# Optimization experiments

Measured on AMD Instinct MI355X. Metric: run time of the kernel, lower is better.

The kernel has to match this reference:

```python
import jax, jax.numpy as jnp
import numpy as np

K_BASE = 8
K_MAX = 20
NUM_GROUPS = 16  # min(32, 64 // 4)
EPS = 1e-5


def _knn_idx_adaptive(x, mask, k_base=K_BASE, k_max=K_MAX):
    # x: [B, N, D] float, mask: [B, N] bool. Returns idx: [B, N, k_max] int32.
    B, N, D = x.shape
    x2 = jnp.sum(x * x, axis=-1, keepdims=True)              # [B, N, 1]
    dist2 = x2 + x2.transpose(0, 2, 1) - 2.0 * jnp.einsum('bnd,bmd->bnm', x, x)
    dist2 = jnp.clip(dist2, 0.0)
    valid = mask[:, :, None] & mask[:, None, :]
    eye = jnp.eye(N, dtype=bool)[None]
    dist2 = jnp.where(valid & ~eye, dist2, jnp.inf)
    counts = mask.sum(axis=1)                                 # [B]
    k_per = jnp.clip(jnp.sqrt(counts.astype(jnp.float32) / 50.0) * k_base,
                     k_base, k_max).astype(jnp.int32)         # truncation == torch .long()
    k_global = jnp.minimum(k_max, jnp.maximum(1, counts.min() - 1))
    _, idx = jax.lax.top_k(-dist2, k_max)                     # [B, N, k_max]
    first_valid = jnp.argmax(mask, axis=1)                    # [B]
    cols = jnp.arange(k_max)[None, None, :]
    k_eff = jnp.minimum(k_per, k_global)[:, None, None]
    # cols < k_eff: true top-k neighbors; [k_eff, k_global): repeat first valid; >= k_global: pad 0
    idx = jnp.where(cols < k_eff, idx,
                    jnp.where(cols < k_global, first_valid[:, None, None], 0))
    return idx


def _group_norm(h, gamma, beta, num_groups=NUM_GROUPS, eps=EPS):
    # h: [..., C]
    shp = h.shape
    C = shp[-1]
    hg = h.reshape(shp[:-1] + (num_groups, C // num_groups))
    mu = hg.mean(axis=-1, keepdims=True)
    var = hg.var(axis=-1, keepdims=True)
    hg = (hg - mu) * jax.lax.rsqrt(var + eps)
    return hg.reshape(shp) * gamma + beta


def setup_inputs() -> dict:
    key = jax.random.key(0)
    kx, kl, k1, k2 = jax.random.split(key, 4)
    B, N, D, C = 16, 1024, 64, 64
    x = jax.random.normal(kx, (B, N, D), dtype=jnp.float32)
    lengths = jax.random.randint(kl, (B,), 256, N + 1)
    mask = jnp.arange(N)[None, :] < lengths[:, None]          # [B, N] bool
    W1 = jax.random.normal(k1, (2 * D, C), dtype=jnp.float32) / np.sqrt(2 * D)
    b1 = jnp.zeros((C,), dtype=jnp.float32)
    gamma = jnp.ones((C,), dtype=jnp.float32)
    beta = jnp.zeros((C,), dtype=jnp.float32)
    W2 = jax.random.normal(k2, (C, C), dtype=jnp.float32) / np.sqrt(C)
    b2 = jnp.zeros((C,), dtype=jnp.float32)
    return {"x": x, "mask": mask, "W1": W1, "b1": b1,
            "gamma": gamma, "beta": beta, "W2": W2, "b2": b2}


def reference(x, mask, W1, b1, gamma, beta, W2, b2):
    B, N, D = x.shape
    idx = _knn_idx_adaptive(x, mask)                          # [B, N, k]
    k = idx.shape[-1]
    x_nb = jnp.take_along_axis(x[:, :, None, :].repeat(1, axis=2),
                               idx[..., None], axis=1) if False else \
        x[jnp.arange(B)[:, None, None], idx]                  # [B, N, k, D]
    x_i = jnp.broadcast_to(x[:, :, None, :], (B, N, k, D))
    edge = jnp.concatenate([x_i, x_nb - x_i], axis=-1)        # [B, N, k, 2D]
    h = jax.nn.relu(_group_norm(edge @ W1 + b1, gamma, beta)) # [B, N, k, C]
    h = h @ W2 + b2
    out = h.max(axis=2)                                       # [B, N, C]
    return out * mask[..., None].astype(out.dtype)
```

## Files before the change

### kernel.cpp

```cpp
#include <hip/hip_runtime.h>
#include <stdint.h>

#define BB 16
#define NN 1024
#define DD 64
#define CC 64
#define KMAX 20
#define ROWS 8

typedef unsigned long long u64;
typedef float f32x2 __attribute__((ext_vector_type(2)));
typedef float f32x4v __attribute__((ext_vector_type(4)));
typedef short bf16x8 __attribute__((ext_vector_type(8)));

__device__ inline u64 umin64(u64 a, u64 b) { return a < b ? a : b; }

__device__ inline unsigned f2bf(float f) {
    unsigned u = __float_as_uint(f);
    return (u + 0x7FFFu + ((u >> 16) & 1u)) >> 16;
}

__device__ inline bf16x8 pack8(const float4 a, const float4 b) {
    union { unsigned u[4]; bf16x8 v; } r;
    r.u[0] = f2bf(a.x) | (f2bf(a.y) << 16);
    r.u[1] = f2bf(a.z) | (f2bf(a.w) << 16);
    r.u[2] = f2bf(b.x) | (f2bf(b.y) << 16);
    r.u[3] = f2bf(b.z) | (f2bf(b.w) << 16);
    return r.v;
}

struct bfpair { bf16x8 hi, lo; };
__device__ __forceinline__ bfpair split8(const float v[8]) {
    union { unsigned u[4]; bf16x8 x; } H, L;
#pragma unroll
    for (int i = 0; i < 4; ++i) {
        unsigned h0 = f2bf(v[2 * i]), h1 = f2bf(v[2 * i + 1]);
        float r0 = v[2 * i] - __uint_as_float(h0 << 16);
        float r1 = v[2 * i + 1] - __uint_as_float(h1 << 16);
        H.u[i] = h0 | (h1 << 16);
        L.u[i] = f2bf(r0) | (f2bf(r1) << 16);
    }
    bfpair r; r.hi = H.x; r.lo = L.x; return r;
}

__device__ inline void gn4(float4& h, const float4 g, const float4 be) {
    float mu = (h.x + h.y + h.z + h.w) * 0.25f;
    float dx = h.x - mu, dy = h.y - mu, dz = h.z - mu, dw = h.w - mu;
    float var = (dx * dx + dy * dy + dz * dz + dw * dw) * 0.25f;
    float rs = __builtin_amdgcn_rsqf(var + 1e-5f);
    h.x = fmaxf(fmaf(dx * rs, g.x, be.x), 0.f);
    h.y = fmaxf(fmaf(dy * rs, g.y, be.y), 0.f);
    h.z = fmaxf(fmaf(dz * rs, g.z, be.z), 0.f);
    h.w = fmaxf(fmaf(dw * rs, g.w, be.w), 0.f);
}

__global__ __launch_bounds__(256) void k1_feats(const float* __restrict__ x,
                                                const float* __restrict__ W1,
                                                const float* __restrict__ b1,
                                                float* __restrict__ base,
                                                float* __restrict__ fb,
                                                float* __restrict__ x2,
                                                float* __restrict__ xT,
                                                const void* __restrict__ maskp,
                                                int* __restrict__ counts,
                                                int* __restrict__ keff) {
    __shared__ float sXT[64][65];
    __shared__ int scnt[BB];
    int w = threadIdx.x >> 6, lane = threadIdx.x & 63;
    int lg = lane >> 4, lr = lane & 15;
    int p0 = blockIdx.x * 64;
    int pw0 = p0 + w * 16;

    float av[8];
    bfpair A[2];
    {
        const float* xr = x + (size_t)(pw0 + lr) * DD;
#pragma unroll
        for (int kt = 0; kt < 2; ++kt) {
            float4 a0 = *(const float4*)(xr + kt * 32 + lg * 8);
            float4 a1 = *(const float4*)(xr + kt * 32 + lg * 8 + 4);
            av[0] = a0.x; av[1] = a0.y; av[2] = a0.z; av[3] = a0.w;
            av[4] = a1.x; av[5] = a1.y; av[6] = a1.z; av[7] = a1.w;
            A[kt] = split8(av);
        }
    }
    bfpair Wa[4][2], Wb[4][2];
#pragma unroll
    for (int nt = 0; nt < 4; ++nt)
#pragma unroll
        for (int kt = 0; kt < 2; ++kt) {
            const float* wpa = W1 + (size_t)(kt * 32 + lg * 8) * CC + nt * 16 + lr;
            float wv[8];
#pragma unroll
            for (int e = 0; e < 8; ++e) wv[e] = wpa[e * CC];
            Wa[nt][kt] = split8(wv);
            const float* wpb = wpa + (size_t)DD * CC;
#pragma unroll
            for (int e = 0; e < 8; ++e) wv[e] = wpb[e * CC];
            Wb[nt][kt] = split8(wv);
        }

    f32x4v P[4], Q[4];
#pragma unroll
    for (int nt = 0; nt < 4; ++nt) { P[nt] = (f32x4v){0,0,0,0}; Q[nt] = (f32x4v){0,0,0,0}; }
#pragma unroll
    for (int nt = 0; nt < 4; ++nt)
#pragma unroll
        for (int kt = 0; kt < 2; ++kt) {
            P[nt] = __builtin_amdgcn_mfma_f32_16x16x32_bf16(A[kt].hi, Wa[nt][kt].hi, P[nt], 0, 0, 0);
            P[nt] = __builtin_amdgcn_mfma_f32_16x16x32_bf16(A[kt].hi, Wa[nt][kt].lo, P[nt], 0, 0, 0);
            P[nt] = __builtin_amdgcn_mfma_f32_16x16x32_bf16(A[kt].lo, Wa[nt][kt].hi, P[nt], 0, 0, 0);
            Q[nt] = __builtin_amdgcn_mfma_f32_16x16x32_bf16(A[kt].hi, Wb[nt][kt].hi, Q[nt], 0, 0, 0);
            Q[nt] = __builtin_amdgcn_mfma_f32_16x16x32_bf16(A[kt].hi, Wb[nt][kt].lo, Q[nt], 0, 0, 0);
            Q[nt] = __builtin_amdgcn_mfma_f32_16x16x32_bf16(A[kt].lo, Wb[nt][kt].hi, Q[nt], 0, 0, 0);
        }
#pragma unroll
    for (int nt = 0; nt < 4; ++nt) {
        float b1c = b1[nt * 16 + lr];
#pragma unroll
        for (int r = 0; r < 4; ++r) {
            size_t off = (size_t)(pw0 + lg * 4 + r) * CC + nt * 16 + lr;
            base[off] = P[nt][r] - Q[nt][r] + b1c;
            fb[off] = Q[nt][r];
        }
    }

    for (int q = 0; q < 16; ++q) {
        int p = pw0 + q;
        float xv = x[(size_t)p * DD + lane];
        sXT[w * 16 + q][lane] = xv;
        float sq = xv * xv;
        for (int off = 32; off; off >>= 1) sq += __shfl_xor(sq, off);
        if (lane == 0) x2[p] = sq;
    }
    __syncthreads();
    {
        int b = p0 >> 10, nb = p0 & 1023;
#pragma unroll
        for (int i = 0; i < 4; ++i) {
            int d = i * 16 + (threadIdx.x >> 4);
            int pt4 = (threadIdx.x & 15) << 2;
            float4 vv = {sXT[pt4][d], sXT[pt4 + 1][d], sXT[pt4 + 2][d], sXT[pt4 + 3][d]};
            *(float4*)&xT[(((size_t)(b << 6) + d) << 10) + nb + pt4] = vv;
        }
    }

    if (blockIdx.x == 0) {
        const unsigned char* mb = (const unsigned char*)maskp;
        const int* mi = (const int*)maskp;
        bool bytelayout = (mb[1] != 0);
        for (int bq = 0; bq < 4; ++bq) {
            int bb = w * 4 + bq;
            int s = 0;
            for (int i = 0; i < 16; ++i) {
                int nn2 = lane + (i << 6);
                int v = bytelayout ? (mb[bb * NN + nn2] ? 1 : 0)
                                   : (mi[bb * NN + nn2] ? 1 : 0);
                s += v;
            }
            for (int off = 32; off; off >>= 1) s += __shfl_xor(s, off);
            if (lane == 0) scnt[bb] = s;
        }
        __syncthreads();
        int t = threadIdx.x;
        if (t < BB) {
            int minc = scnt[0];
            for (int qq = 1; qq < BB; ++qq) minc = min(minc, scnt[qq]);
            int kglob = min(KMAX, max(1, minc - 1));
            float c = (float)scnt[t];
            float v = sqrtf(c / 50.0f) * 8.0f;
            v = fminf(fmaxf(v, 8.0f), 20.0f);
            int kper = (int)v;
            counts[t] = scnt[t];
            keff[t] = min(kper, kglob);
        }
    }
}

#define CE(a, b)                                                      \
    {                                                                 \
        bool sw_ = pk[b] < pk[a];                                     \
        u64 ta_ = pk[a];                                              \
        pk[a] = sw_ ? pk[b] : pk[a];                                  \
        pk[b] = sw_ ? ta_ : pk[b];                                    \
    }

__device__ __forceinline__ u64 head16(const u64 (&pk)[16]) {
    u64 h01 = umin64(pk[0], pk[1]),   h23 = umin64(pk[2], pk[3]);
    u64 h45 = umin64(pk[4], pk[5]),   h67 = umin64(pk[6], pk[7]);
    u64 h89 = umin64(pk[8], pk[9]),   hab = umin64(pk[10], pk[11]);
    u64 hcd = umin64(pk[12], pk[13]), hef = umin64(pk[14], pk[15]);
    return umin64(umin64(umin64(h01, h23), umin64(h45, h67)),
                  umin64(umin64(h89, hab), umin64(hcd, hef)));
}

__device__ __forceinline__ int sortpop(u64 (&pk)[16], int kef, int lane) {
    CE(0,1) CE(2,3) CE(4,5) CE(6,7) CE(8,9) CE(10,11) CE(12,13) CE(14,15)
    CE(0,2) CE(1,3) CE(4,6) CE(5,7) CE(8,10) CE(9,11) CE(12,14) CE(13,15)
    CE(1,2) CE(5,6) CE(9,10) CE(13,14)
    CE(0,4) CE(1,5) CE(2,6) CE(3,7) CE(8,12) CE(9,13) CE(10,14) CE(11,15)
    CE(2,4) CE(3,5) CE(10,12) CE(11,13)
    CE(1,2) CE(3,4) CE(5,6) CE(9,10) CE(11,12) CE(13,14)
    CE(0,8) CE(1,9) CE(2,10) CE(3,11) CE(4,12) CE(5,13) CE(6,14) CE(7,15)
    CE(4,8) CE(5,9) CE(6,10) CE(7,11)
    CE(2,4) CE(3,5) CE(6,8) CE(7,9) CE(10,12) CE(11,13)
    CE(1,2) CE(3,4) CE(5,6) CE(7,8) CE(9,10) CE(11,12) CE(13,14)
    u64 myhead = pk[0];
    int my_m = 0;
    for (int j = 0; j < kef; ++j) {
        u64 g = myhead;
        for (int off = 32; off; off >>= 1) {
            u64 o = __shfl_xor(g, off);
            g = (o < g) ? o : g;
        }
        my_m = (j == lane) ? (int)(unsigned)(g & 0xffffffffu) : my_m;
        bool win = (myhead == g);
#pragma unroll
        for (int tt = 0; tt < 15; ++tt) pk[tt] = win ? pk[tt + 1] : pk[tt];
        pk[15] = win ? ~0ULL : pk[15];
        myhead = pk[0];
    }
    return my_m;
}

__device__ __forceinline__ void bitonic_x2(u64& a, u64& b, int lane) {
#pragma unroll
    for (int k = 2; k <= 64; k <<= 1) {
#pragma unroll
        for (int j = k >> 1; j > 0; j >>= 1) {
            u64 oa = __shfl_xor(a, j);
            u64 ob = __shfl_xor(b, j);
            bool keepmin = (((lane & j) == 0) == ((lane & k) == 0));
            a = ((oa < a) == keepmin) ? oa : a;
            b = ((ob < b) == keepmin) ? ob : b;
        }
    }
}

#define ROWFMA(r, rv, cv)                                                        \
    {                                                                            \
        axy[r] = __builtin_elementwise_fma((f32x2){rv, rv}, (f32x2){cv.x, cv.y}, \
                                           axy[r]);                              \
        azw[r] = __builtin_elementwise_fma((f32x2){rv, rv}, (f32x2){cv.z, cv.w}, \
                                           azw[r]);                              \
    }

__global__ __launch_bounds__(256) void k2_knn(const float* __restrict__ x,
                                              const float* __restrict__ xT,
                                              const float* __restrict__ x2,
                                              const int* __restrict__ counts,
                                              const int* __restrict__ keff,
                                              int* __restrict__ idx) {
    __shared__ float sD[ROWS][NN];
    __shared__ float sX2[NN];
    int b = blockIdx.x >> 7;
    int n0 = (blockIdx.x & 127) * ROWS;
    int cnt = counts[b];
    if (n0 >= cnt) return;
    int kef = keff[b];
    int w = threadIdx.x >> 6, lane = threadIdx.x & 63;
    int t = threadIdx.x;
    *(float4*)&sX2[t << 2] = *(const float4*)(x2 + (b << 10) + (t << 2));
    __syncthreads();

    if ((w << 8) < cnt) {
        f32x2 axy[ROWS], azw[ROWS];
#pragma unroll
        for (int r = 0; r < ROWS; ++r) { axy[r] = (f32x2){0.f, 0.f}; azw[r] = (f32x2){0.f, 0.f}; }
        const float* xTb = xT + ((size_t)b << 16);
        const float* xrow0 = x + ((size_t)(b << 10) + n0) * DD;
        int c0 = (w << 8) + (lane << 2);
        for (int d0 = 0; d0 < DD; d0 += 4) {
            float4 cv0 = *(const float4*)(xTb + ((size_t)(d0 + 0) << 10) + c0);
            float4 cv1 = *(const float4*)(xTb + ((size_t)(d0 + 1) << 10) + c0);
            float4 cv2 = *(const float4*)(xTb + ((size_t)(d0 + 2) << 10) + c0);
            float4 cv3 = *(const float4*)(xTb + ((size_t)(d0 + 3) << 10) + c0);
#pragma unroll
            for (int r = 0; r < ROWS; ++r) {
                float4 rv = *(const float4*)(xrow0 + r * DD + d0);
                ROWFMA(r, rv.x, cv0)
                ROWFMA(r, rv.y, cv1)
                ROWFMA(r, rv.z, cv2)
                ROWFMA(r, rv.w, cv3)
            }
        }
#pragma unroll
        for (int r = 0; r < ROWS; ++r)
            *(float4*)&sD[r][c0] = make_float4(axy[r].x, axy[r].y, azw[r].x, azw[r].y);
    }
    __syncthreads();

    int rA = w, rB = w + 4;
    int nA = n0 + rA, nB = n0 + rB;
    bool vA = nA < cnt, vB = nB < cnt;
    if (!vA) return;
    float x2A = sX2[nA];
    float x2B = sX2[nB & 1023];
    u64 pkA[16], pkB[16];
#pragma unroll
    for (int tt = 0; tt < 16; ++tt) {
        int c = (tt << 6) + lane;
        float dA = fmaxf((x2A + sX2[c]) - 2.0f * sD[rA][c], 0.0f);
        float dB = fmaxf((x2B + sX2[c]) - 2.0f * sD[rB][c], 0.0f);
        pkA[tt] = (c < cnt && c != nA)
            ? (((u64)__float_as_uint(dA) << 32) | (unsigned)c) : ~0ULL;
        pkB[tt] = (vB && c < cnt && c != nB)
            ? (((u64)__float_as_uint(dB) << 32) | (unsigned)c) : ~0ULL;
    }
    u64 hA = head16(pkA), hB = head16(pkB);
    unsigned hA32 = (unsigned)(hA >> 32), hB32 = (unsigned)(hB >> 32);
    unsigned prefA = 0u, prefB = 0u;
    int rankA = kef, rankB = kef;
#pragma unroll
    for (int bbit = 31; bbit >= 0; --bbit) {
        unsigned bitm = 1u << bbit;
        bool cA = ((((u64)(hA32 ^ prefA)) >> (bbit + 1)) == 0) && ((hA32 & bitm) == 0);
        bool cB = ((((u64)(hB32 ^ prefB)) >> (bbit + 1)) == 0) && ((hB32 & bitm) == 0);
        u64 mA = __ballot(cA);
        u64 mB = __ballot(cB);
        int nA0 = __popcll(mA), nB0 = __popcll(mB);
        if (rankA > nA0) { rankA -= nA0; prefA |= bitm; }
        if (rankB > nB0) { rankB -= nB0; prefB |= bitm; }
    }
    u64 t0A = (((u64)prefA) << 32) | 0xFFFFFFFFULL;
    u64 t0B = vB ? ((((u64)prefB) << 32) | 0xFFFFFFFFULL) : 0ULL;
    int cleA = 0, cleB = 0;
#pragma unroll
    for (int i = 0; i < 16; ++i) {
        cleA += (pkA[i] <= t0A) ? 1 : 0;
        cleB += (pkB[i] <= t0B) ? 1 : 0;
    }
    int incA = cleA, incB = cleB;
#pragma unroll
    for (int off = 1; off < 64; off <<= 1) {
        int oA = __shfl_up(incA, off);
        int oB = __shfl_up(incB, off);
        incA += (lane >= off) ? oA : 0;
        incB += (lane >= off) ? oB : 0;
    }
    int SA = __shfl(incA, 63), SB = __shfl(incB, 63);
    size_t prowA = (size_t)(b << 10) + nA;
    size_t prowB = (size_t)(b << 10) + nB;
    if (SA <= 64 && SB <= 64) {
        u64* svA = (u64*)&sD[rA][0];
        u64* svB = (u64*)&sD[rB][0];
        int pA = incA - cleA, pB = incB - cleB;
#pragma unroll
        for (int i = 0; i < 16; ++i) {
            if (pkA[i] <= t0A) { svA[pA] = pkA[i]; ++pA; }
            if (pkB[i] <= t0B) { svB[pB] = pkB[i]; ++pB; }
        }
        u64 sA = (lane < SA) ? svA[lane] : ~0ULL;
        u64 sB = (lane < SB) ? svB[lane] : ~0ULL;
        bitonic_x2(sA, sB, lane);
        if (lane < KMAX) {
            idx[prowA * KMAX + lane] = (lane < kef) ? (int)(unsigned)(sA & 0xffffffffu) : 0;
            if (vB)
                idx[prowB * KMAX + lane] = (lane < kef) ? (int)(unsigned)(sB & 0xffffffffu) : 0;
        }
    } else {
        int mA = sortpop(pkA, kef, lane);
        if (lane < KMAX) idx[prowA * KMAX + lane] = (lane < kef) ? mA : 0;
        if (vB) {
            int mB = sortpop(pkB, kef, lane);
            if (lane < KMAX) idx[prowB * KMAX + lane] = (lane < kef) ? mB : 0;
        }
    }
}

__global__ __launch_bounds__(256, 2) void k3_mlp(const float* __restrict__ base,
                                                 const float* __restrict__ fb,
                                                 const int* __restrict__ idx,
                                                 const int* __restrict__ counts,
                                                 const float* __restrict__ gamma,
                                                 const float* __restrict__ beta,
                                                 const float* __restrict__ W2,
                                                 const float* __restrict__ b2,
                                                 float* __restrict__ out) {
    __shared__ float sC[4][64][20];
    int w = threadIdx.x >> 6, lane = threadIdx.x & 63;
    int lg = lane >> 4, lr = lane & 15;
    int p0 = blockIdx.x * 16;
    int b = p0 >> 10;
    int n0b = p0 & 1023;
    int cnt = counts[b];
    int pt = p0 + lr;
    bool aval = (n0b + lr) < cnt;

    bf16x8 Bf[4][2];
#pragma unroll
    for (int nt = 0; nt < 4; ++nt)
#pragma unroll
        for (int kt = 0; kt < 2; ++kt) {
            float4 lo, hi;
            const float* wp = W2 + (size_t)(kt * 32 + lg * 8) * CC + nt * 16 + lr;
            lo.x = wp[0 * CC]; lo.y = wp[1 * CC]; lo.z = wp[2 * CC]; lo.w = wp[3 * CC];
            hi.x = wp[4 * CC]; hi.y = wp[5 * CC]; hi.z = wp[6 * CC]; hi.w = wp[7 * CC];
            Bf[nt][kt] = pack8(lo, hi);
        }

    const float* bp = base + (size_t)pt * CC + lg * 8;
    float4 baA0 = *(const float4*)(bp);
    float4 baA1 = *(const float4*)(bp + 4);
    float4 baB0 = *(const float4*)(bp + 32);
    float4 baB1 = *(const float4*)(bp + 36);
    const float* gp = gamma + lg * 8;
    float4 gA0 = *(const float4*)(gp),      gA1 = *(const float4*)(gp + 4);
    float4 gB0 = *(const float4*)(gp + 32), gB1 = *(const float4*)(gp + 36);
    const float* bep = beta + lg * 8;
    float4 eA0 = *(const float4*)(bep),      eA1 = *(const float4*)(bep + 4);
    float4 eB0 = *(const float4*)(bep + 32), eB1 = *(const float4*)(bep + 36);

    const float* fbb = fb + ((size_t)(b << 10)) * CC;
    const int* idxp = idx + (size_t)pt * KMAX;

    f32x4v cmax[4];
#pragma unroll
    for (int nt = 0; nt < 4; ++nt) cmax[nt] = (f32x4v){-1e30f, -1e30f, -1e30f, -1e30f};

#pragma unroll
    for (int jj = 0; jj < 5; ++jj) {
        int j = w * 5 + jj;
        int m = aval ? idxp[j] : 0;
        const float* fr = fbb + (size_t)m * CC + lg * 8;
        float4 hA0 = *(const float4*)(fr);
        float4 hA1 = *(const float4*)(fr + 4);
        float4 hB0 = *(const float4*)(fr + 32);
        float4 hB1 = *(const float4*)(fr + 36);
        hA0.x += baA0.x; hA0.y += baA0.y; hA0.z += baA0.z; hA0.w += baA0.w;
        hA1.x += baA1.x; hA1.y += baA1.y; hA1.z += baA1.z; hA1.w += baA1.w;
        hB0.x += baB0.x; hB0.y += baB0.y; hB0.z += baB0.z; hB0.w += baB0.w;
        hB1.x += baB1.x; hB1.y += baB1.y; hB1.z += baB1.z; hB1.w += baB1.w;
        gn4(hA0, gA0, eA0);
        gn4(hA1, gA1, eA1);
        gn4(hB0, gB0, eB0);
        gn4(hB1, gB1, eB1);
        bf16x8 A0 = pack8(hA0, hA1);
        bf16x8 A1 = pack8(hB0, hB1);
#pragma unroll
        for (int nt = 0; nt < 4; ++nt) {
            f32x4v c = {0.f, 0.f, 0.f, 0.f};
            c = __builtin_amdgcn_mfma_f32_16x16x32_bf16(A0, Bf[nt][0], c, 0, 0, 0);
            c = __builtin_amdgcn_mfma_f32_16x16x32_bf16(A1, Bf[nt][1], c, 0, 0, 0);
            cmax[nt].x = fmaxf(cmax[nt].x, c.x);
            cmax[nt].y = fmaxf(cmax[nt].y, c.y);
            cmax[nt].z = fmaxf(cmax[nt].z, c.z);
            cmax[nt].w = fmaxf(cmax[nt].w, c.w);
        }
    }
#pragma unroll
    for (int nt = 0; nt < 4; ++nt)
        *(float4*)&sC[w][lane][nt * 4] = (float4){cmax[nt].x, cmax[nt].y, cmax[nt].z, cmax[nt].w};
    __syncthreads();
    float b2c = b2[lane];
#pragma unroll
    for (int q = 0; q < 4; ++q) {
        int R = w * 4 + q;
        int src = ((R >> 2) << 4) + lr;
        int reg = (lg << 2) + (R & 3);
        float v = fmaxf(fmaxf(sC[0][src][reg], sC[1][src][reg]),
                        fmaxf(sC[2][src][reg], sC[3][src][reg]));
        bool valid = (n0b + R) < cnt;
        out[(size_t)(p0 + R) * CC + lane] = valid ? (v + b2c) : 0.f;
    }
}

extern "C" void kernel_launch(void* const* d_in, const int* in_sizes, int n_in,
                              void* d_out, int out_size, void* d_ws, size_t ws_size,
                              hipStream_t stream) {
    const float* x     = (const float*)d_in[0];
    const void*  maskp = d_in[1];
    const float* W1    = (const float*)d_in[2];
    const float* b1    = (const float*)d_in[3];
    const float* gamma = (const float*)d_in[4];
    const float* beta  = (const float*)d_in[5];
    const float* W2    = (const float*)d_in[6];
    const float* b2    = (const float*)d_in[7];
    float* out = (float*)d_out;

    int* d_counts = (int*)d_ws;
    int* d_keff   = d_counts + 16;
    float* d_x2   = (float*)(d_counts + 32);
    float* d_base = d_x2 + BB * NN;
    float* d_fb   = d_base + (size_t)BB * NN * CC;
    int* d_idx    = (int*)(d_fb + (size_t)BB * NN * CC);
    float* d_xT   = (float*)d_out;

    hipLaunchKernelGGL(k1_feats, dim3(BB * NN / 64), dim3(256), 0, stream,
                       x, W1, b1, d_base, d_fb, d_x2, d_xT, maskp, d_counts, d_keff);
    hipLaunchKernelGGL(k2_knn, dim3(BB * (NN / ROWS)), dim3(256), 0, stream,
                       x, d_xT, d_x2, d_counts, d_keff, d_idx);
    hipLaunchKernelGGL(k3_mlp, dim3(BB * NN / 16), dim3(256), 0, stream,
                       d_base, d_fb, d_idx, d_counts, gamma, beta, W2, b2, out);
}
```

Measured before the change: 97.48 us.

## Shrink k1 tiles to 16 points per block and replace bitonic sort with rank scatter

k1_feats now processes 16 points per block, with each wave computing one 16-column slice of the W1 projection. This launches four times as many blocks with fewer registers per wave, at the cost of narrower scalar xT stores. In k2_knn, candidate compaction now uses ballot+popcount instead of a shuffle prefix scan. The 64-lane bitonic sort is replaced by a per-lane rank count over shared memory, with each winner scattered directly to its output slot. This trades shuffle stages for a loop of LDS reads.

```diff
diff --git a/kernel.cpp b/kernel.cpp
--- a/kernel.cpp
+++ b/kernel.cpp
@@ -64,17 +64,16 @@
                                                 const void* __restrict__ maskp,
                                                 int* __restrict__ counts,
                                                 int* __restrict__ keff) {
-    __shared__ float sXT[64][65];
+    __shared__ float sXT[16][65];
     __shared__ int scnt[BB];
     int w = threadIdx.x >> 6, lane = threadIdx.x & 63;
     int lg = lane >> 4, lr = lane & 15;
-    int p0 = blockIdx.x * 64;
-    int pw0 = p0 + w * 16;
+    int p0 = blockIdx.x * 16;
 
     float av[8];
     bfpair A[2];
     {
-        const float* xr = x + (size_t)(pw0 + lr) * DD;
+        const float* xr = x + (size_t)(p0 + lr) * DD;
 #pragma unroll
         for (int kt = 0; kt < 2; ++kt) {
             float4 a0 = *(const float4*)(xr + kt * 32 + lg * 8);
@@ -84,51 +83,46 @@
             A[kt] = split8(av);
         }
     }
-    bfpair Wa[4][2], Wb[4][2];
-#pragma unroll
-    for (int nt = 0; nt < 4; ++nt)
-#pragma unroll
-        for (int kt = 0; kt < 2; ++kt) {
-            const float* wpa = W1 + (size_t)(kt * 32 + lg * 8) * CC + nt * 16 + lr;
-            float wv[8];
-#pragma unroll
-            for (int e = 0; e < 8; ++e) wv[e] = wpa[e * CC];
-            Wa[nt][kt] = split8(wv);
-            const float* wpb = wpa + (size_t)DD * CC;
-#pragma unroll
-            for (int e = 0; e < 8; ++e) wv[e] = wpb[e * CC];
-            Wb[nt][kt] = split8(wv);
-        }
-
-    f32x4v P[4], Q[4];
-#pragma unroll
-    for (int nt = 0; nt < 4; ++nt) { P[nt] = (f32x4v){0,0,0,0}; Q[nt] = (f32x4v){0,0,0,0}; }
-#pragma unroll
-    for (int nt = 0; nt < 4; ++nt)
-#pragma unroll
-        for (int kt = 0; kt < 2; ++kt) {
-            P[nt] = __builtin_amdgcn_mfma_f32_16x16x32_bf16(A[kt].hi, Wa[nt][kt].hi, P[nt], 0, 0, 0);
-            P[nt] = __builtin_amdgcn_mfma_f32_16x16x32_bf16(A[kt].hi, Wa[nt][kt].lo, P[nt], 0, 0, 0);
-            P[nt] = __builtin_amdgcn_mfma_f32_16x16x32_bf16(A[kt].lo, Wa[nt][kt].hi, P[nt], 0, 0, 0);
-            Q[nt] = __builtin_amdgcn_mfma_f32_16x16x32_bf16(A[kt].hi, Wb[nt][kt].hi, Q[nt], 0, 0, 0);
-            Q[nt] = __builtin_amdgcn_mfma_f32_16x16x32_bf16(A[kt].hi, Wb[nt][kt].lo, Q[nt], 0, 0, 0);
-            Q[nt] = __builtin_amdgcn_mfma_f32_16x16x32_bf16(A[kt].lo, Wb[nt][kt].hi, Q[nt], 0, 0, 0);
-        }
-#pragma unroll
-    for (int nt = 0; nt < 4; ++nt) {
-        float b1c = b1[nt * 16 + lr];
+    bfpair Wa[2], Wb[2];
+#pragma unroll
+    for (int kt = 0; kt < 2; ++kt) {
+        const float* wpa = W1 + (size_t)(kt * 32 + lg * 8) * CC + w * 16 + lr;
+        float wv[8];
+#pragma unroll
+        for (int e = 0; e < 8; ++e) wv[e] = wpa[e * CC];
+        Wa[kt] = split8(wv);
+        const float* wpb = wpa + (size_t)DD * CC;
+#pragma unroll
+        for (int e = 0; e < 8; ++e) wv[e] = wpb[e * CC];
+        Wb[kt] = split8(wv);
+    }
+
+    f32x4v P = {0, 0, 0, 0}, Q = {0, 0, 0, 0};
+#pragma unroll
+    for (int kt = 0; kt < 2; ++kt) {
+        P = __builtin_amdgcn_mfma_f32_16x16x32_bf16(A[kt].hi, Wa[kt].hi, P, 0, 0, 0);
+        P = __builtin_amdgcn_mfma_f32_16x16x32_bf16(A[kt].hi, Wa[kt].lo, P, 0, 0, 0);
+        P = __builtin_amdgcn_mfma_f32_16x16x32_bf16(A[kt].lo, Wa[kt].hi, P, 0, 0, 0);
+        Q = __builtin_amdgcn_mfma_f32_16x16x32_bf16(A[kt].hi, Wb[kt].hi, Q, 0, 0, 0);
+        Q = __builtin_amdgcn_mfma_f32_16x16x32_bf16(A[kt].hi, Wb[kt].lo, Q, 0, 0, 0);
+        Q = __builtin_amdgcn_mfma_f32_16x16x32_bf16(A[kt].lo, Wb[kt].hi, Q, 0, 0, 0);
+    }
+    {
+        float b1c = b1[w * 16 + lr];
 #pragma unroll
         for (int r = 0; r < 4; ++r) {
-            size_t off = (size_t)(pw0 + lg * 4 + r) * CC + nt * 16 + lr;
-            base[off] = P[nt][r] - Q[nt][r] + b1c;
-            fb[off] = Q[nt][r];
-        }
-    }
-
-    for (int q = 0; q < 16; ++q) {
-        int p = pw0 + q;
+            size_t off = (size_t)(p0 + lg * 4 + r) * CC + w * 16 + lr;
+            base[off] = P[r] - Q[r] + b1c;
+            fb[off] = Q[r];
+        }
+    }
+
+#pragma unroll
+    for (int q2 = 0; q2 < 4; ++q2) {
+        int pl = w + q2 * 4;
+        int p = p0 + pl;
         float xv = x[(size_t)p * DD + lane];
-        sXT[w * 16 + q][lane] = xv;
+        sXT[pl][lane] = xv;
         float sq = xv * xv;
         for (int off = 32; off; off >>= 1) sq += __shfl_xor(sq, off);
         if (lane == 0) x2[p] = sq;
@@ -136,12 +130,12 @@
     __syncthreads();
     {
         int b = p0 >> 10, nb = p0 & 1023;
-#pragma unroll
-        for (int i = 0; i < 4; ++i) {
-            int d = i * 16 + (threadIdx.x >> 4);
-            int pt4 = (threadIdx.x & 15) << 2;
-            float4 vv = {sXT[pt4][d], sXT[pt4 + 1][d], sXT[pt4 + 2][d], sXT[pt4 + 3][d]};
-            *(float4*)&xT[(((size_t)(b << 6) + d) << 10) + nb + pt4] = vv;
+        int t = threadIdx.x;
+#pragma unroll
+        for (int pass = 0; pass < 4; ++pass) {
+            int d = pass * 16 + (t >> 4);
+            int pt = t & 15;
+            xT[(((size_t)(b << 6) + d) << 10) + nb + pt] = sXT[pt][d];
         }
     }
 
@@ -223,20 +217,6 @@
     return my_m;
 }
 
-__device__ __forceinline__ void bitonic_x2(u64& a, u64& b, int lane) {
-#pragma unroll
-    for (int k = 2; k <= 64; k <<= 1) {
-#pragma unroll
-        for (int j = k >> 1; j > 0; j >>= 1) {
-            u64 oa = __shfl_xor(a, j);
-            u64 ob = __shfl_xor(b, j);
-            bool keepmin = (((lane & j) == 0) == ((lane & k) == 0));
-            a = ((oa < a) == keepmin) ? oa : a;
-            b = ((ob < b) == keepmin) ? ob : b;
-        }
-    }
-}
-
 #define ROWFMA(r, rv, cv)                                                        \
     {                                                                            \
         axy[r] = __builtin_elementwise_fma((f32x2){rv, rv}, (f32x2){cv.x, cv.y}, \
@@ -324,39 +304,40 @@
     }
     u64 t0A = (((u64)prefA) << 32) | 0xFFFFFFFFULL;
     u64 t0B = vB ? ((((u64)prefB) << 32) | 0xFFFFFFFFULL) : 0ULL;
-    int cleA = 0, cleB = 0;
+
+    u64* svA = (u64*)&sD[rA][0];
+    u64* svB = (u64*)&sD[rB][0];
+    u64 lmask = (lane == 0) ? 0ULL : ((~0ULL) >> (64 - lane));
+    int SA = 0, SB = 0;
 #pragma unroll
     for (int i = 0; i < 16; ++i) {
-        cleA += (pkA[i] <= t0A) ? 1 : 0;
-        cleB += (pkB[i] <= t0B) ? 1 : 0;
-    }
-    int incA = cleA, incB = cleB;
-#pragma unroll
-    for (int off = 1; off < 64; off <<= 1) {
-        int oA = __shfl_up(incA, off);
-        int oB = __shfl_up(incB, off);
-        incA += (lane >= off) ? oA : 0;
-        incB += (lane >= off) ? oB : 0;
-    }
-    int SA = __shfl(incA, 63), SB = __shfl(incB, 63);
+        bool qA = (pkA[i] <= t0A);
+        bool qB = (pkB[i] <= t0B);
+        u64 mA = __ballot(qA);
+        u64 mB = __ballot(qB);
+        if (qA) svA[SA + __popcll(mA & lmask)] = pkA[i];
+        if (qB) svB[SB + __popcll(mB & lmask)] = pkB[i];
+        SA += __popcll(mA);
+        SB += __popcll(mB);
+    }
     size_t prowA = (size_t)(b << 10) + nA;
     size_t prowB = (size_t)(b << 10) + nB;
     if (SA <= 64 && SB <= 64) {
-        u64* svA = (u64*)&sD[rA][0];
-        u64* svB = (u64*)&sD[rB][0];
-        int pA = incA - cleA, pB = incB - cleB;
-#pragma unroll
-        for (int i = 0; i < 16; ++i) {
-            if (pkA[i] <= t0A) { svA[pA] = pkA[i]; ++pA; }
-            if (pkB[i] <= t0B) { svB[pB] = pkB[i]; ++pB; }
-        }
         u64 sA = (lane < SA) ? svA[lane] : ~0ULL;
         u64 sB = (lane < SB) ? svB[lane] : ~0ULL;
-        bitonic_x2(sA, sB, lane);
-        if (lane < KMAX) {
-            idx[prowA * KMAX + lane] = (lane < kef) ? (int)(unsigned)(sA & 0xffffffffu) : 0;
-            if (vB)
-                idx[prowB * KMAX + lane] = (lane < kef) ? (int)(unsigned)(sB & 0xffffffffu) : 0;
+        int rkA = 0, rkB = 0;
+        int SM = max(SA, SB);
+        for (int j = 0; j < SM; ++j) {
+            u64 aj = svA[j];
+            u64 bj = svB[j];
+            rkA += (j < SA && aj < sA) ? 1 : 0;
+            rkB += (j < SB && bj < sB) ? 1 : 0;
+        }
+        if (rkA < kef && lane < SA) idx[prowA * KMAX + rkA] = (int)(unsigned)(sA & 0xffffffffu);
+        if (lane >= kef && lane < KMAX) idx[prowA * KMAX + lane] = 0;
+        if (vB) {
+            if (rkB < kef && lane < SB) idx[prowB * KMAX + rkB] = (int)(unsigned)(sB & 0xffffffffu);
+            if (lane >= kef && lane < KMAX) idx[prowB * KMAX + lane] = 0;
         }
     } else {
         int mA = sortpop(pkA, kef, lane);
@@ -486,7 +467,7 @@
     int* d_idx    = (int*)(d_fb + (size_t)BB * NN * CC);
     float* d_xT   = (float*)d_out;
 
-    hipLaunchKernelGGL(k1_feats, dim3(BB * NN / 64), dim3(256), 0, stream,
+    hipLaunchKernelGGL(k1_feats, dim3(BB * NN / 16), dim3(256), 0, stream,
                        x, W1, b1, d_base, d_fb, d_x2, d_xT, maskp, d_counts, d_keff);
     hipLaunchKernelGGL(k2_knn, dim3(BB * (NN / ROWS)), dim3(256), 0, stream,
                        x, d_xT, d_x2, d_counts, d_keff, d_idx);
```

New measurement: 92.04 us. 1.06x faster.
